# Performance work log

Hardware: AMD Instinct MI355X
Metric: run time of the kernel (lower is better)

## Reference

```python
import jax, jax.numpy as jnp
import numpy as np

KH, KW = 3, 3   # kernel_size
DH, DW = 2, 2   # stride


def _extract_windows(x):
    """Equivalent of x.unfold(2,KH,DH).unfold(3,KW,DW).view(B,C,H',W',KH*KW).
    Loop is over the KH*KW=9 fixed kernel offsets, not data dims."""
    B, C, H, W = x.shape
    Ho = (H - KH) // DH + 1
    Wo = (W - KW) // DW + 1
    cols = [x[:, :, i:i + DH * Ho:DH, j:j + DW * Wo:DW]
            for i in range(KH) for j in range(KW)]  # row-major (kh,kw) matches torch unfold flatten
    return jnp.stack(cols, axis=-1)  # (B, C, Ho, Wo, KH*KW)


def setup_inputs() -> dict:
    key = jax.random.key(0)
    k1, k2 = jax.random.split(key)
    x = jax.random.normal(k1, (8, 32, 64, 64), dtype=jnp.float32)
    # weight: (1, out_channels, in_channels, H', W', kh*kw) with H'=W'=31
    weight = jax.random.normal(k2, (1, 32, 32, 31, 31, 9), dtype=jnp.float32)
    return {"x": x, "weight": weight}


def reference(x, weight):
    # windows: (B, in, H', W', K); weight[0]: (out, in, H', W', K)
    # out[b,o,p,q] = sum_{i,k} windows[b,i,p,q,k] * weight[0,o,i,p,q,k]
    windows = _extract_windows(x)
    return jnp.einsum('bipqk,oipqk->bopq', windows, weight[0])
```

## Files before the change

kernel.cpp:

```cpp
#include <hip/hip_runtime.h>


#define CIN 32
#define COUT 32
#define HH 64
#define WW 64
#define HO 31
#define WO 31
#define XB 131072

__global__ __launch_bounds__(512) void lc2d_kernel(const float* __restrict__ x,
                                                   const float* __restrict__ wgt,
                                                   float* __restrict__ out) {
    const int t = threadIdx.x;
    const int qlane = t & 31;
    const int ic = t >> 5;
    const int p  = blockIdx.x >> 4;
    const int og = blockIdx.x & 15;
    const int q  = (qlane < 31) ? qlane : 30;
    const int o0 = og * 2;

    float acc[2][8];
#pragma unroll
    for (int lo = 0; lo < 2; ++lo)
#pragma unroll
        for (int b = 0; b < 8; ++b) acc[lo][b] = 0.f;

    const int pq9 = (p * WO + q) * 9;

#pragma unroll
    for (int ii = 0; ii < 2; ++ii) {
        const int i = ic * 2 + ii;

        float wv[2][9];
#pragma unroll
        for (int lo = 0; lo < 2; ++lo) {
            const float* wp = wgt + ((size_t)((o0 + lo) * CIN + i) * (HO * WO) + p * WO + q) * 9;
#pragma unroll
            for (int k = 0; k < 9; ++k) wv[lo][k] = __builtin_nontemporal_load(wp + k);
        }

#pragma unroll
        for (int kh = 0; kh < 3; ++kh) {
            const float* xr = x + ((size_t)i * HH + (2 * p + kh)) * WW + 2 * q;
            float xk[8][3];
#pragma unroll
            for (int b = 0; b < 8; ++b) {
                const float* xb = xr + (size_t)b * XB;
                const float2 a = *reinterpret_cast<const float2*>(xb);
                const float2 c = *reinterpret_cast<const float2*>(xb + 2);
                xk[b][0] = a.x; xk[b][1] = a.y; xk[b][2] = c.x;
            }
#pragma unroll
            for (int lo = 0; lo < 2; ++lo)
#pragma unroll
                for (int b = 0; b < 8; ++b)
#pragma unroll
                    for (int kw = 0; kw < 3; ++kw)
                        acc[lo][b] += wv[lo][kh * 3 + kw] * xk[b][kw];
        }
    }

    __shared__ float red[16][32][17];
#pragma unroll
    for (int lo = 0; lo < 2; ++lo)
#pragma unroll
        for (int b = 0; b < 8; ++b)
            red[ic][qlane][lo * 8 + b] = acc[lo][b];
    __syncthreads();

    if (t < 496) {
        const int qq = t % 31;
        const int e  = t / 31;
        float s = 0.f;
#pragma unroll
        for (int icc = 0; icc < 16; ++icc) s += red[icc][qq][e];
        const int lo = e >> 3, b = e & 7;
        out[(((size_t)b * COUT + o0 + lo) * HO + p) * WO + qq] = s;
    }
}

extern "C" void kernel_launch(void* const* d_in, const int* in_sizes, int n_in,
                              void* d_out, int out_size, void* d_ws, size_t ws_size,
                              hipStream_t stream) {
    const float* x = (const float*)d_in[0];
    const float* w = (const float*)d_in[1];
    float* out = (float*)d_out;
    lc2d_kernel<<<dim3(HO * 16), dim3(512), 0, stream>>>(x, w, out);
}
```

Before: 93.01 us.

## Stage weight rows through LDS with async global_load_lds and union smem

Weights are now fetched cooperatively as contiguous per-row segments using global_load_lds into shared memory, so each (o,i,p) row of 279 floats is read coalesced rather than as strided 9-float per-thread reads. The input-channel loop is split into two halves with barriers, and the shared weight buffer is unioned with the reduction buffer. Launch bounds now request 4 blocks per CU and the FMA loop is restructured. This adds extra barriers and LDS traffic, and clamps off-segment lanes to duplicate loads.

New measurement: 116.7 us. +25.5%, slower.

```diff
diff --git a/kernel.cpp b/kernel.cpp
--- a/kernel.cpp
+++ b/kernel.cpp
@@ -8,10 +8,23 @@
 #define HO 31
 #define WO 31
 #define XB 131072
+#define WSEG 279
+#define WPAD 288
+#define WOI 8649
 
-__global__ __launch_bounds__(512) void lc2d_kernel(const float* __restrict__ x,
-                                                   const float* __restrict__ wgt,
-                                                   float* __restrict__ out) {
+#define GLD_LDS(gp, lp)                                              \
+    __builtin_amdgcn_global_load_lds(                                \
+        (const __attribute__((address_space(1))) void*)(gp),         \
+        (__attribute__((address_space(3))) void*)(lp), 4, 0, 0)
+
+__global__ __launch_bounds__(512, 4) void lc2d_kernel(const float* __restrict__ x,
+                                                      const float* __restrict__ wgt,
+                                                      float* __restrict__ out) {
+    __shared__ union {
+        float w[32 * WPAD];
+        float red[16][32][17];
+    } sm;
+
     const int t = threadIdx.x;
     const int qlane = t & 31;
     const int ic = t >> 5;
@@ -26,55 +39,68 @@
 #pragma unroll
         for (int b = 0; b < 8; ++b) acc[lo][b] = 0.f;
 
-    const int pq9 = (p * WO + q) * 9;
+    const float* xq = x + 2 * q;
+    const int ldsWaveBase = t & ~63;
+
+    for (int h = 0; h < 2; ++h) {
+        if (h) __syncthreads();
 
 #pragma unroll
-    for (int ii = 0; ii < 2; ++ii) {
-        const int i = ic * 2 + ii;
+        for (int j = 0; j < 18; ++j) {
+            const int f = t + j * 512;
+            const int u = f >> 5;
+            const int seg = u / 9;
+            int off = f - seg * WPAD;
+            if (off > WSEG - 1) off = WSEG - 1;
+            const int oi = o0 * CIN + h * 16 + seg + (seg & 16);
+            const float* gp = wgt + (size_t)oi * WOI + p * WSEG + off;
+            GLD_LDS(gp, &sm.w[j * 512 + ldsWaveBase]);
+        }
+        __syncthreads();
 
+        const int i = h * 16 + ic;
         float wv[2][9];
+        const int wb0 = ic * WPAD + q * 9;
+        const int wb1 = (16 + ic) * WPAD + q * 9;
 #pragma unroll
-        for (int lo = 0; lo < 2; ++lo) {
-            const float* wp = wgt + ((size_t)((o0 + lo) * CIN + i) * (HO * WO) + p * WO + q) * 9;
-#pragma unroll
-            for (int k = 0; k < 9; ++k) wv[lo][k] = __builtin_nontemporal_load(wp + k);
+        for (int k = 0; k < 9; ++k) {
+            wv[0][k] = sm.w[wb0 + k];
+            wv[1][k] = sm.w[wb1 + k];
         }
 
+        const float* xrow0 = xq + ((size_t)i * HH + 2 * p) * WW;
 #pragma unroll
         for (int kh = 0; kh < 3; ++kh) {
-            const float* xr = x + ((size_t)i * HH + (2 * p + kh)) * WW + 2 * q;
-            float xk[8][3];
+            const float* xr = xrow0 + kh * WW;
 #pragma unroll
             for (int b = 0; b < 8; ++b) {
                 const float* xb = xr + (size_t)b * XB;
                 const float2 a = *reinterpret_cast<const float2*>(xb);
                 const float2 c = *reinterpret_cast<const float2*>(xb + 2);
-                xk[b][0] = a.x; xk[b][1] = a.y; xk[b][2] = c.x;
+#pragma unroll
+                for (int lo = 0; lo < 2; ++lo)
+                    acc[lo][b] += wv[lo][kh * 3 + 0] * a.x
+                                + wv[lo][kh * 3 + 1] * a.y
+                                + wv[lo][kh * 3 + 2] * c.x;
             }
-#pragma unroll
-            for (int lo = 0; lo < 2; ++lo)
-#pragma unroll
-                for (int b = 0; b < 8; ++b)
-#pragma unroll
-                    for (int kw = 0; kw < 3; ++kw)
-                        acc[lo][b] += wv[lo][kh * 3 + kw] * xk[b][kw];
         }
     }
 
-    __shared__ float red[16][32][17];
+    __syncthreads();
+
 #pragma unroll
     for (int lo = 0; lo < 2; ++lo)
 #pragma unroll
         for (int b = 0; b < 8; ++b)
-            red[ic][qlane][lo * 8 + b] = acc[lo][b];
+            sm.red[ic][qlane][lo * 8 + b] = acc[lo][b];
     __syncthreads();
 
     if (t < 496) {
-        const int qq = t % 31;
         const int e  = t / 31;
+        const int qq = t - e * 31;
         float s = 0.f;
 #pragma unroll
-        for (int icc = 0; icc < 16; ++icc) s += red[icc][qq][e];
+        for (int icc = 0; icc < 16; ++icc) s += sm.red[icc][qq][e];
         const int lo = e >> 3, b = e & 7;
         out[(((size_t)b * COUT + o0 + lo) * HO + p) * WO + qq] = s;
     }
```
